# Optimization experiments

Measured on AMD Instinct MI355X. Metric: run time of the kernel, lower is better.

## Reference

```python
import jax, jax.numpy as jnp
import numpy as np

IN_DIM = 128
SLOT_SIZE = 64
NUM_SLOTS = 8
NUM_ITERS = 3
MLP_HDIM = 128
EPSILON = 1e-08


def _layernorm(x, g, b, eps=1e-5):
    m = jnp.mean(x, axis=-1, keepdims=True)
    v = jnp.mean((x - m) ** 2, axis=-1, keepdims=True)
    return (x - m) * jax.lax.rsqrt(v + eps) * g + b


def setup_inputs() -> dict:
    key = jax.random.key(0)
    ks = jax.random.split(key, 16)
    H, D, K, M = SLOT_SIZE, IN_DIM, NUM_SLOTS, MLP_HDIM
    x = jax.random.normal(ks[0], (32, 4096, D), dtype=jnp.float32)
    noise = jax.random.normal(ks[1], (32, K, H), dtype=jnp.float32)
    s = lambda k, shape, fan_in: jax.random.normal(k, shape, jnp.float32) * (1.0 / np.sqrt(fan_in))
    return {
        'x': x,
        'noise': noise,
        'Wq': s(ks[2], (H, H), H),            # project_q (no bias)
        'Wk': s(ks[3], (H, D), D),            # project_k
        'Wv': s(ks[4], (H, D), D),            # project_v
        'ln_in_g': jnp.ones((D,), jnp.float32), 'ln_in_b': jnp.zeros((D,), jnp.float32),
        'ln_sl_g': jnp.ones((H,), jnp.float32), 'ln_sl_b': jnp.zeros((H,), jnp.float32),
        'ln_mlp_g': jnp.ones((H,), jnp.float32), 'ln_mlp_b': jnp.zeros((H,), jnp.float32),
        'gru_w_ih': s(ks[5], (3 * H, H), H),  # PyTorch GRUCell weight_ih (r,z,n)
        'gru_w_hh': s(ks[6], (3 * H, H), H),
        'gru_b_ih': jnp.zeros((3 * H,), jnp.float32),
        'gru_b_hh': jnp.zeros((3 * H,), jnp.float32),
        'mlp_w1': s(ks[7], (M, H), H), 'mlp_b1': jnp.zeros((M,), jnp.float32),
        'mlp_w2': s(ks[8], (H, M), M), 'mlp_b2': jnp.zeros((H,), jnp.float32),
        'slots_mu': jnp.tile(jnp.linspace(-1.0, 1.0, K, dtype=jnp.float32)[None, :, None], (1, 1, H)),
        'slots_logsigma': jnp.full((1, K, H), -1.0, dtype=jnp.float32),
    }


def reference(x, noise, Wq, Wk, Wv, ln_in_g, ln_in_b, ln_sl_g, ln_sl_b,
              ln_mlp_g, ln_mlp_b, gru_w_ih, gru_w_hh, gru_b_ih, gru_b_hh,
              mlp_w1, mlp_b1, mlp_w2, mlp_b2, slots_mu, slots_logsigma):
    B = x.shape[0]
    H, K = SLOT_SIZE, NUM_SLOTS
    xn = _layernorm(x, ln_in_g, ln_in_b)
    k = jnp.einsum('bnd,hd->bnh', xn, Wk)  # [B,N,H]
    v = jnp.einsum('bnd,hd->bnh', xn, Wv)

    scale = jax.nn.softplus(slots_logsigma) + 1e-05
    slots = slots_mu + scale * noise  # rsample, broadcast over batch -> [B,K,H]

    def step(slots):
        slots_prev = slots
        s = _layernorm(slots, ln_sl_g, ln_sl_b)
        q = jnp.einsum('bkh,gh->bkg', s, Wq)  # [B,K,H]
        scores = (H ** -0.5) * jnp.einsum('bnh,bkh->bnk', k, q)
        attn = jax.nn.softmax(scores, axis=-1) + EPSILON  # softmax over slots
        attn = attn / jnp.sum(attn, axis=1, keepdims=True)  # normalize over inputs
        updates = jnp.einsum('bnk,bnh->bkh', attn, v)
        # PyTorch GRUCell: gates ordered (r, z, n)
        u = updates.reshape(-1, H)
        h = slots_prev.reshape(-1, H)
        gx = u @ gru_w_ih.T + gru_b_ih
        gh = h @ gru_w_hh.T + gru_b_hh
        xr, xz, xn_ = jnp.split(gx, 3, axis=-1)
        hr, hz, hn = jnp.split(gh, 3, axis=-1)
        r = jax.nn.sigmoid(xr + hr)
        z = jax.nn.sigmoid(xz + hz)
        n = jnp.tanh(xn_ + r * hn)
        slots = ((1.0 - z) * n + z * h).reshape(B, K, H)
        slots = _layernorm(slots, ln_mlp_g, ln_mlp_b)
        mlp_out = jax.nn.relu(slots @ mlp_w1.T + mlp_b1) @ mlp_w2.T + mlp_b2
        return slots + mlp_out

    for _ in range(NUM_ITERS):
        slots = step(slots)
    return slots
```

## Files before the change

kernel.cpp:

```cpp
#include <hip/hip_runtime.h>

typedef __attribute__((ext_vector_type(8))) short s16x8;
typedef __attribute__((ext_vector_type(4))) float f32x4;

#define DEV static __device__ __forceinline__

DEV float b2f(unsigned short u){
  unsigned int i = ((unsigned int)u) << 16;
  float f; __builtin_memcpy(&f, &i, 4); return f;
}
DEV unsigned short f2b(float f){
  unsigned int i; __builtin_memcpy(&i, &f, 4);
  i = i + 0x7fffu + ((i >> 16) & 1u);
  return (unsigned short)(i >> 16);
}
DEV f32x4 mfma16(s16x8 a, s16x8 b, f32x4 c){
  return __builtin_amdgcn_mfma_f32_16x16x32_bf16(a, b, c, 0, 0, 0);
}
DEV s16x8 ld8f(const float* p){
  const float4* q4 = (const float4*)p;
  float4 a = q4[0], b = q4[1];
  s16x8 r;
  r[0]=(short)f2b(a.x); r[1]=(short)f2b(a.y); r[2]=(short)f2b(a.z); r[3]=(short)f2b(a.w);
  r[4]=(short)f2b(b.x); r[5]=(short)f2b(b.y); r[6]=(short)f2b(b.z); r[7]=(short)f2b(b.w);
  return r;
}

template<int C> DEV float dpp_addstep(float x){
  int y = __builtin_amdgcn_update_dpp(0, __builtin_bit_cast(int, x), C, 0xF, 0xF, true);
  return x + __builtin_bit_cast(float, y);
}
DEV float rsum16(float v){
  v = dpp_addstep<0xB1>(v);
  v = dpp_addstep<0x4E>(v);
  v = dpp_addstep<0x141>(v);
  v = dpp_addstep<0x140>(v);
  return v;
}

__global__ __launch_bounds__(256) void k_wpack(
    const float* __restrict__ Wk, const float* __restrict__ Wv,
    unsigned short* __restrict__ wkb, unsigned short* __restrict__ wvb)
{
  int t = blockIdx.x * 256 + threadIdx.x;
  const float* src = (t < 2048) ? (Wk + t*4) : (Wv + (t-2048)*4);
  unsigned short* dst = (t < 2048) ? (wkb + t*4) : (wvb + (t-2048)*4);
  float4 v = *(const float4*)src;
  ushort4 o;
  o.x = f2b(v.x); o.y = f2b(v.y); o.z = f2b(v.z); o.w = f2b(v.w);
  *(ushort4*)dst = o;
}

__global__ __launch_bounds__(256, 4) void k_lnkv(
    const float* __restrict__ x,
    const unsigned short* __restrict__ wkb,
    const unsigned short* __restrict__ wvb,
    const float* __restrict__ lg,
    const float* __restrict__ lb,
    unsigned short* __restrict__ kg,
    unsigned short* __restrict__ vt)
{
  __shared__ unsigned int xs[128 * 68];
  const int tid = threadIdx.x;
  const int w = tid >> 6, ln = tid & 63;
  const int m16 = ln & 15, q = ln >> 4;
  const int b = blockIdx.x >> 5;
  const int nbase = (blockIdx.x & 31) << 7;
  const long rowg0 = (long)b * 4096 + nbase;

  {
    const int c = m16;
    const float4 gA = *(const float4*)(lg + c*4);
    const float4 gB = *(const float4*)(lg + 64 + c*4);
    const float4 bA = *(const float4*)(lb + c*4);
    const float4 bB = *(const float4*)(lb + 64 + c*4);
    const float* base = x + (rowg0 + w*32 + q)*128;

    float4 va[2], vb[2];
    va[0] = *(const float4*)(base + c*4);
    vb[0] = *(const float4*)(base + 64 + c*4);
    #pragma unroll
    for (int p = 0; p < 8; ++p){
      const int cur = p & 1, nxt = cur ^ 1;
      if (p < 7){
        va[nxt] = *(const float4*)(base + (p+1)*512 + c*4);
        vb[nxt] = *(const float4*)(base + (p+1)*512 + 64 + c*4);
      }
      float4 u = va[cur], t = vb[cur];
      float s1 = (u.x + u.y) + (u.z + u.w) + (t.x + t.y) + (t.z + t.w);
      float s2 = (u.x*u.x + u.y*u.y) + (u.z*u.z + u.w*u.w)
               + (t.x*t.x + t.y*t.y) + (t.z*t.z + t.w*t.w);
      s1 = rsum16(s1);
      s2 = rsum16(s2);
      float mean = s1 * (1.f/128.f);
      float var  = s2 * (1.f/128.f) - mean*mean;
      float rs = rsqrtf(var + 1e-5f);
      float y0 = (u.x - mean)*rs*gA.x + bA.x;
      float y1 = (u.y - mean)*rs*gA.y + bA.y;
      float y2 = (u.z - mean)*rs*gA.z + bA.z;
      float y3 = (u.w - mean)*rs*gA.w + bA.w;
      float y4 = (t.x - mean)*rs*gB.x + bB.x;
      float y5 = (t.y - mean)*rs*gB.y + bB.y;
      float y6 = (t.z - mean)*rs*gB.z + bB.z;
      float y7 = (t.w - mean)*rs*gB.w + bB.w;
      uint2 pkA, pkB;
      pkA.x = (unsigned int)f2b(y0) | ((unsigned int)f2b(y1) << 16);
      pkA.y = (unsigned int)f2b(y2) | ((unsigned int)f2b(y3) << 16);
      pkB.x = (unsigned int)f2b(y4) | ((unsigned int)f2b(y5) << 16);
      pkB.y = (unsigned int)f2b(y6) | ((unsigned int)f2b(y7) << 16);
      const int r = w*32 + p*4 + q;
      *(uint2*)&xs[r*68 + c*2] = pkA;
      *(uint2*)&xs[r*68 + 32 + c*2] = pkB;
    }
  }

  s16x8 bw[4][4];
  #pragma unroll
  for (int t = 0; t < 4; ++t)
    #pragma unroll
    for (int kb = 0; kb < 4; ++kb)
      bw[kb][t] = *(const s16x8*)(wkb + (t*16 + m16)*128 + kb*32 + q*8);

  __syncthreads();

  const f32x4 zf = {0.f, 0.f, 0.f, 0.f};

  #pragma unroll
  for (int mi = 0; mi < 2; ++mi){
    int n0 = (w*2 + mi) * 16;
    f32x4 acc[4];
    #pragma unroll
    for (int t = 0; t < 4; ++t) acc[t] = zf;
    #pragma unroll
    for (int kb = 0; kb < 4; ++kb){
      s16x8 af = *(const s16x8*)((const unsigned short*)(xs + (n0 + m16)*68) + kb*32 + q*8);
      #pragma unroll
      for (int t = 0; t < 4; ++t)
        acc[t] = mfma16(af, bw[kb][t], acc[t]);
    }
    #pragma unroll
    for (int t = 0; t < 4; ++t){
      int h = t*16 + m16;
      #pragma unroll
      for (int rr = 0; rr < 4; ++rr){
        long n = rowg0 + n0 + q*4 + rr;
        kg[n*64 + h] = f2b(acc[t][rr]);
      }
    }
  }

  #pragma unroll
  for (int t = 0; t < 4; ++t)
    #pragma unroll
    for (int kb = 0; kb < 4; ++kb)
      bw[kb][t] = *(const s16x8*)(wvb + (t*16 + m16)*128 + kb*32 + q*8);

  #pragma unroll
  for (int mi = 0; mi < 2; ++mi){
    int n0 = (w*2 + mi) * 16;
    f32x4 acc[4];
    #pragma unroll
    for (int t = 0; t < 4; ++t) acc[t] = zf;
    #pragma unroll
    for (int kb = 0; kb < 4; ++kb){
      s16x8 af = *(const s16x8*)((const unsigned short*)(xs + (n0 + m16)*68) + kb*32 + q*8);
      #pragma unroll
      for (int t = 0; t < 4; ++t)
        acc[t] = mfma16(af, bw[kb][t], acc[t]);
    }
    #pragma unroll
    for (int t = 0; t < 4; ++t){
      int h = t*16 + m16;
      unsigned int p0 = (unsigned int)f2b(acc[t][0]) | ((unsigned int)f2b(acc[t][1]) << 16);
      unsigned int p1 = (unsigned int)f2b(acc[t][2]) | ((unsigned int)f2b(acc[t][3]) << 16);
      uint2 pv; pv.x = p0; pv.y = p1;
      long off = ((long)b*64 + h)*4096 + nbase + n0 + q*4;
      *(uint2*)(vt + off) = pv;
    }
  }
}

__global__ __launch_bounds__(256) void k_init2(
    const float* __restrict__ noise,
    const float* __restrict__ mu,
    const float* __restrict__ lsg,
    const float* __restrict__ gsl,
    const float* __restrict__ bsl,
    const float* __restrict__ Wq,
    float* __restrict__ slots,
    unsigned short* __restrict__ qws,
    float* __restrict__ U, float* __restrict__ S)
{
  __shared__ unsigned short st[16*72];
  __shared__ __align__(16) float redS[16][4];
  __shared__ __align__(16) float redQ[16][4];
  const int tid = threadIdx.x;
  const int w = tid >> 6, ln = tid & 63;
  const int m16 = ln & 15, q = ln >> 4;
  const int r0 = blockIdx.x * 16;
  const int cw = w*16 + m16;

  float sl[4], s1[4], s2[4];
  #pragma unroll
  for (int rr = 0; rr < 4; ++rr){
    int row = r0 + q*4 + rr;
    int k = row & 7;
    float v = mu[k*64 + cw] + (log1pf(expf(lsg[k*64 + cw])) + 1e-5f) * noise[row*64 + cw];
    sl[rr] = v;
    slots[row*64 + cw] = v;
    s1[rr] = v; s2[rr] = v*v;
  }
  #pragma unroll
  for (int m = 1; m < 16; m <<= 1){
    #pragma unroll
    for (int rr = 0; rr < 4; ++rr){
      s1[rr] += __shfl_xor(s1[rr], m);
      s2[rr] += __shfl_xor(s2[rr], m);
    }
  }
  if (m16 == 0){
    #pragma unroll
    for (int rr = 0; rr < 4; ++rr){ redS[q*4+rr][w] = s1[rr]; redQ[q*4+rr][w] = s2[rr]; }
  }
  __syncthreads();
  {
    const float gs = gsl[cw], bs = bsl[cw];
    #pragma unroll
    for (int rr = 0; rr < 4; ++rr){
      f32x4 aS = *(const f32x4*)redS[q*4+rr];
      f32x4 aQ = *(const f32x4*)redQ[q*4+rr];
      float tS = aS[0]+aS[1]+aS[2]+aS[3];
      float tQ = aQ[0]+aQ[1]+aQ[2]+aQ[3];
      float mean = tS*(1.f/64.f);
      float var  = tQ*(1.f/64.f) - mean*mean;
      float rs = rsqrtf(var + 1e-5f);
      float sq = (sl[rr] - mean)*rs*gs + bs;
      st[(q*4+rr)*72 + cw] = f2b(sq);
    }
  }
  __syncthreads();
  {
    f32x4 acc = {0,0,0,0};
    #pragma unroll
    for (int ks = 0; ks < 2; ++ks){
      s16x8 a = *(const s16x8*)(st + m16*72 + ks*32 + q*8);
      acc = mfma16(a, ld8f(Wq + cw*64 + ks*32 + q*8), acc);
    }
    #pragma unroll
    for (int rr = 0; rr < 4; ++rr){
      int row = r0 + q*4 + rr;
      int bb_ = row >> 3, kk = row & 7;
      qws[(bb_*16 + kk)*64 + cw] = f2b(acc[rr] * 0.125f);
    }
  }
  {
    f32x4 z = {0,0,0,0};
    *(f32x4*)(U + r0*64 + tid*4) = z;
    if (tid < 16) S[r0 + tid] = 0.f;
    int b0 = blockIdx.x * 2;
    ((unsigned int*)(qws + (b0*16 + 8)*64))[tid] = 0u;
    ((unsigned int*)(qws + ((b0+1)*16 + 8)*64))[tid] = 0u;
  }
}

__global__ __launch_bounds__(256) void k_attn(
    const unsigned short* __restrict__ kg,
    const unsigned short* __restrict__ vt,
    const unsigned short* __restrict__ qws,
    float* __restrict__ U, float* __restrict__ S)
{
  __shared__ float sc[256*17];
  __shared__ unsigned short aT[16*264];
  const int tid = threadIdx.x;
  const int w = tid >> 6, ln = tid & 63;
  const int m16 = ln & 15, q = ln >> 4;
  const int b = blockIdx.x >> 4;
  const int nbase = (blockIdx.x & 15) << 8;

  for (int i = tid; i < 8*264; i += 256) aT[8*264 + i] = 0;

  s16x8 bq[2];
  #pragma unroll
  for (int ks = 0; ks < 2; ++ks)
    bq[ks] = *(const s16x8*)(qws + (b*16 + m16)*64 + ks*32 + q*8);

  #pragma unroll
  for (int mi = 0; mi < 4; ++mi){
    int n0 = (w*4 + mi)*16;
    f32x4 acc = {0.f, 0.f, 0.f, 0.f};
    #pragma unroll
    for (int ks = 0; ks < 2; ++ks){
      s16x8 af = *(const s16x8*)(kg + ((long)b*4096 + nbase + n0 + m16)*64 + ks*32 + q*8);
      acc = mfma16(af, bq[ks], acc);
    }
    #pragma unroll
    for (int rr = 0; rr < 4; ++rr)
      sc[(n0 + q*4 + rr)*17 + m16] = acc[rr];
  }
  __syncthreads();

  {
    int r = tid;
    float a8[8];
    float mx = -1e30f;
    #pragma unroll
    for (int j = 0; j < 8; ++j){ a8[j] = sc[r*17 + j]; mx = fmaxf(mx, a8[j]); }
    float ssum = 0.f;
    #pragma unroll
    for (int j = 0; j < 8; ++j){ a8[j] = expf(a8[j] - mx); ssum += a8[j]; }
    float inv = 1.f/ssum;
    #pragma unroll
    for (int j = 0; j < 8; ++j)
      aT[j*264 + r] = f2b(a8[j]*inv + 1e-8f);
  }
  __syncthreads();

  {
    int j = tid >> 5, c = tid & 31;
    float p = 0.f;
    #pragma unroll
    for (int i = 0; i < 8; ++i) p += b2f(aT[j*264 + c + 32*i]);
    #pragma unroll
    for (int m = 16; m >= 1; m >>= 1) p += __shfl_xor(p, m);
    if ((ln & 31) == 0) atomicAdd(&S[b*8 + j], p);
  }

  {
    f32x4 acc = {0.f, 0.f, 0.f, 0.f};
    #pragma unroll
    for (int ks = 0; ks < 8; ++ks){
      s16x8 af = *(const s16x8*)(aT + m16*264 + ks*32 + q*8);
      s16x8 bf = *(const s16x8*)(vt + ((long)b*64 + w*16 + m16)*4096 + nbase + ks*32 + q*8);
      acc = mfma16(af, bf, acc);
    }
    #pragma unroll
    for (int rr = 0; rr < 4; ++rr){
      int slot = q*4 + rr;
      if (slot < 8)
        atomicAdd(&U[b*512 + slot*64 + w*16 + m16], acc[rr]);
    }
  }
}

__global__ __launch_bounds__(256) void k_gru(
    const float* __restrict__ U, const float* __restrict__ S,
    float* __restrict__ slots,
    const float* __restrict__ wih, const float* __restrict__ whh,
    const float* __restrict__ bih, const float* __restrict__ bhh,
    const float* __restrict__ w1, const float* __restrict__ b1p,
    const float* __restrict__ w2, const float* __restrict__ b2p,
    const float* __restrict__ gmlp, const float* __restrict__ bmlp,
    const float* __restrict__ gsl, const float* __restrict__ bsl,
    const float* __restrict__ Wq,
    unsigned short* __restrict__ qws,
    float* __restrict__ outp,
    float* __restrict__ Uz, float* __restrict__ Sz)
{
  __shared__ unsigned short ut[16*72], ht[16*72], st[16*72], hid[16*136];
  __shared__ __align__(16) float redS[16][4];
  __shared__ __align__(16) float redQ[16][4];
  const int tid = threadIdx.x;
  const int w = tid >> 6, ln = tid & 63;
  const int m16 = ln & 15, q = ln >> 4;
  const int r0 = blockIdx.x * 16;
  const int cw = w*16 + m16;

  #pragma unroll
  for (int p = 0; p < 4; ++p){
    int row = p*4 + w;
    float sv = S[r0 + row];
    float uu = U[(r0 + row)*64 + ln] / sv;
    ut[row*72 + ln] = f2b(uu);
    ht[row*72 + ln] = f2b(slots[(r0 + row)*64 + ln]);
  }
  __syncthreads();

  f32x4 axr = {0,0,0,0}, axz = {0,0,0,0}, axn = {0,0,0,0};
  f32x4 ahr = {0,0,0,0}, ahz = {0,0,0,0}, ahn = {0,0,0,0};
  #pragma unroll
  for (int ks = 0; ks < 2; ++ks){
    s16x8 au = *(const s16x8*)(ut + m16*72 + ks*32 + q*8);
    s16x8 ah = *(const s16x8*)(ht + m16*72 + ks*32 + q*8);
    axr = mfma16(au, ld8f(wih + (      cw)*64 + ks*32 + q*8), axr);
    axz = mfma16(au, ld8f(wih + ( 64 + cw)*64 + ks*32 + q*8), axz);
    axn = mfma16(au, ld8f(wih + (128 + cw)*64 + ks*32 + q*8), axn);
    ahr = mfma16(ah, ld8f(whh + (      cw)*64 + ks*32 + q*8), ahr);
    ahz = mfma16(ah, ld8f(whh + ( 64 + cw)*64 + ks*32 + q*8), ahz);
    ahn = mfma16(ah, ld8f(whh + (128 + cw)*64 + ks*32 + q*8), ahn);
  }
  const float bxr = bih[cw], bxz = bih[64+cw], bxn = bih[128+cw];
  const float bhr = bhh[cw], bhz = bhh[64+cw], bhn = bhh[128+cw];
  float sp[4];
  #pragma unroll
  for (int rr = 0; rr < 4; ++rr){
    float xr = axr[rr] + bxr, xz = axz[rr] + bxz, xnv = axn[rr] + bxn;
    float hr = ahr[rr] + bhr, hz = ahz[rr] + bhz, hn = ahn[rr] + bhn;
    float rg = 1.f / (1.f + expf(-(xr + hr)));
    float zg = 1.f / (1.f + expf(-(xz + hz)));
    float ng = tanhf(xnv + rg*hn);
    float hv = b2f(ht[(q*4 + rr)*72 + cw]);
    sp[rr] = (1.f - zg)*ng + zg*hv;
  }

  float s1[4], s2[4];
  #pragma unroll
  for (int rr = 0; rr < 4; ++rr){ s1[rr] = sp[rr]; s2[rr] = sp[rr]*sp[rr]; }
  #pragma unroll
  for (int m = 1; m < 16; m <<= 1){
    #pragma unroll
    for (int rr = 0; rr < 4; ++rr){
      s1[rr] += __shfl_xor(s1[rr], m);
      s2[rr] += __shfl_xor(s2[rr], m);
    }
  }
  if (m16 == 0){
    #pragma unroll
    for (int rr = 0; rr < 4; ++rr){ redS[q*4+rr][w] = s1[rr]; redQ[q*4+rr][w] = s2[rr]; }
  }
  __syncthreads();
  float sl_[4];
  {
    const float gm = gmlp[cw], bm = bmlp[cw];
    #pragma unroll
    for (int rr = 0; rr < 4; ++rr){
      f32x4 aS = *(const f32x4*)redS[q*4+rr];
      f32x4 aQ = *(const f32x4*)redQ[q*4+rr];
      float tS = aS[0]+aS[1]+aS[2]+aS[3];
      float tQ = aQ[0]+aQ[1]+aQ[2]+aQ[3];
      float mean = tS*(1.f/64.f);
      float var  = tQ*(1.f/64.f) - mean*mean;
      float rs = rsqrtf(var + 1e-5f);
      sl_[rr] = (sp[rr] - mean)*rs*gm + bm;
      st[(q*4+rr)*72 + cw] = f2b(sl_[rr]);
    }
  }
  __syncthreads();

  #pragma unroll
  for (int t2 = 0; t2 < 2; ++t2){
    int nt = w*2 + t2;
    int col = nt*16 + m16;
    f32x4 acc = {0,0,0,0};
    #pragma unroll
    for (int ks = 0; ks < 2; ++ks){
      s16x8 a = *(const s16x8*)(st + m16*72 + ks*32 + q*8);
      acc = mfma16(a, ld8f(w1 + col*64 + ks*32 + q*8), acc);
    }
    float bb = b1p[col];
    #pragma unroll
    for (int rr = 0; rr < 4; ++rr)
      hid[(q*4+rr)*136 + col] = f2b(fmaxf(acc[rr] + bb, 0.f));
  }
  __syncthreads();

  float snew[4];
  {
    f32x4 acc = {0,0,0,0};
    #pragma unroll
    for (int ks = 0; ks < 4; ++ks){
      s16x8 a = *(const s16x8*)(hid + m16*136 + ks*32 + q*8);
      acc = mfma16(a, ld8f(w2 + cw*128 + ks*32 + q*8), acc);
    }
    float bb = b2p[cw];
    #pragma unroll
    for (int rr = 0; rr < 4; ++rr){
      snew[rr] = sl_[rr] + acc[rr] + bb;
      int row = r0 + q*4 + rr;
      slots[row*64 + cw] = snew[rr];
      outp[row*64 + cw] = snew[rr];
    }
  }

  #pragma unroll
  for (int rr = 0; rr < 4; ++rr){ s1[rr] = snew[rr]; s2[rr] = snew[rr]*snew[rr]; }
  #pragma unroll
  for (int m = 1; m < 16; m <<= 1){
    #pragma unroll
    for (int rr = 0; rr < 4; ++rr){
      s1[rr] += __shfl_xor(s1[rr], m);
      s2[rr] += __shfl_xor(s2[rr], m);
    }
  }
  __syncthreads();
  if (m16 == 0){
    #pragma unroll
    for (int rr = 0; rr < 4; ++rr){ redS[q*4+rr][w] = s1[rr]; redQ[q*4+rr][w] = s2[rr]; }
  }
  __syncthreads();
  {
    const float gs = gsl[cw], bs = bsl[cw];
    #pragma unroll
    for (int rr = 0; rr < 4; ++rr){
      f32x4 aS = *(const f32x4*)redS[q*4+rr];
      f32x4 aQ = *(const f32x4*)redQ[q*4+rr];
      float tS = aS[0]+aS[1]+aS[2]+aS[3];
      float tQ = aQ[0]+aQ[1]+aQ[2]+aQ[3];
      float mean = tS*(1.f/64.f);
      float var  = tQ*(1.f/64.f) - mean*mean;
      float rs = rsqrtf(var + 1e-5f);
      float sq = (snew[rr] - mean)*rs*gs + bs;
      st[(q*4+rr)*72 + cw] = f2b(sq);
    }
  }
  __syncthreads();
  {
    f32x4 acc = {0,0,0,0};
    #pragma unroll
    for (int ks = 0; ks < 2; ++ks){
      s16x8 a = *(const s16x8*)(st + m16*72 + ks*32 + q*8);
      acc = mfma16(a, ld8f(Wq + cw*64 + ks*32 + q*8), acc);
    }
    #pragma unroll
    for (int rr = 0; rr < 4; ++rr){
      int row = r0 + q*4 + rr;
      int bb_ = row >> 3, kk = row & 7;
      qws[(bb_*16 + kk)*64 + cw] = f2b(acc[rr] * 0.125f);
    }
  }
  {
    f32x4 z = {0,0,0,0};
    *(f32x4*)(Uz + r0*64 + tid*4) = z;
    if (tid < 16) Sz[r0 + tid] = 0.f;
    int b0 = blockIdx.x * 2;
    unsigned int* qp0 = (unsigned int*)(qws + (b0*16 + 8)*64);
    unsigned int* qp1 = (unsigned int*)(qws + ((b0+1)*16 + 8)*64);
    qp0[tid] = 0u;
    qp1[tid] = 0u;
  }
}

extern "C" void kernel_launch(void* const* d_in, const int* in_sizes, int n_in,
                              void* d_out, int out_size, void* d_ws, size_t ws_size,
                              hipStream_t stream)
{
  const float* x    = (const float*)d_in[0];
  const float* noise= (const float*)d_in[1];
  const float* Wq   = (const float*)d_in[2];
  const float* Wk   = (const float*)d_in[3];
  const float* Wv   = (const float*)d_in[4];
  const float* ling = (const float*)d_in[5];
  const float* linb = (const float*)d_in[6];
  const float* gsl  = (const float*)d_in[7];
  const float* bsl  = (const float*)d_in[8];
  const float* gmlp = (const float*)d_in[9];
  const float* bmlp = (const float*)d_in[10];
  const float* wih  = (const float*)d_in[11];
  const float* whh  = (const float*)d_in[12];
  const float* bih  = (const float*)d_in[13];
  const float* bhh  = (const float*)d_in[14];
  const float* w1   = (const float*)d_in[15];
  const float* b1p  = (const float*)d_in[16];
  const float* w2   = (const float*)d_in[17];
  const float* b2p  = (const float*)d_in[18];
  const float* mu   = (const float*)d_in[19];
  const float* lsg  = (const float*)d_in[20];

  char* ws = (char*)d_ws;
  unsigned short* kg   = (unsigned short*)(ws);
  unsigned short* vt   = (unsigned short*)(ws + 16777216);
  unsigned short* qws  = (unsigned short*)(ws + 33554432);
  float* slots         = (float*)(ws + 33619968);
  float* U             = (float*)(ws + 33685504);
  float* S             = (float*)(ws + 33751040);
  unsigned short* wkb  = (unsigned short*)(ws + 33752064);
  unsigned short* wvb  = (unsigned short*)(ws + 33768448);
  float* outp          = (float*)d_out;

  hipLaunchKernelGGL(k_wpack, dim3(16), dim3(256), 0, stream, Wk, Wv, wkb, wvb);
  hipLaunchKernelGGL(k_lnkv, dim3(1024), dim3(256), 0, stream, x, wkb, wvb, ling, linb, kg, vt);
  hipLaunchKernelGGL(k_init2, dim3(16), dim3(256), 0, stream, noise, mu, lsg, gsl, bsl, Wq, slots, qws, U, S);
  for (int it = 0; it < 3; ++it){
    hipLaunchKernelGGL(k_attn, dim3(512), dim3(256), 0, stream, kg, vt, qws, U, S);
    hipLaunchKernelGGL(k_gru, dim3(16), dim3(256), 0, stream, U, S, slots,
                       wih, whh, bih, bhh, w1, b1p, w2, b2p, gmlp, bmlp, gsl, bsl, Wq,
                       qws, outp, U, S);
  }
  (void)in_sizes; (void)n_in; (void)out_size; (void)ws_size;
}
```

Measured before the change: 220.0 us.

## Fuse GRU/MLP slot update into attention kernel prologue, drop intermediate GRU launches

Each attention block now recomputes the GRU, MLP, layernorm and q-projection for its batch pair from the previous iteration's U/S accumulators. This replaces the separate 16-block k_gru launches between iterations. Triple-buffered U/S and slot buffers avoid zeroing races, and all small weights are prepacked to bf16 in k_wpack. The trade is redundant per-block compute (32 blocks per batch pair repeat the same work) and extra LDS, in exchange for fewer launches and fewer serial low-occupancy kernels.

Measured after the change: 209.2 us. 1.05x faster.

```diff
diff --git a/kernel.cpp b/kernel.cpp
--- a/kernel.cpp
+++ b/kernel.cpp
@@ -40,11 +40,22 @@
 
 __global__ __launch_bounds__(256) void k_wpack(
     const float* __restrict__ Wk, const float* __restrict__ Wv,
-    unsigned short* __restrict__ wkb, unsigned short* __restrict__ wvb)
+    const float* __restrict__ wih, const float* __restrict__ whh,
+    const float* __restrict__ w1, const float* __restrict__ w2,
+    const float* __restrict__ Wq,
+    unsigned short* __restrict__ wkb, unsigned short* __restrict__ wvb,
+    unsigned short* __restrict__ wall)
 {
   int t = blockIdx.x * 256 + threadIdx.x;
-  const float* src = (t < 2048) ? (Wk + t*4) : (Wv + (t-2048)*4);
-  unsigned short* dst = (t < 2048) ? (wkb + t*4) : (wvb + (t-2048)*4);
+  int off = t * 4;
+  const float* src; unsigned short* dst;
+  if      (off <  8192){ src = Wk  + off;         dst = wkb  + off; }
+  else if (off < 16384){ src = Wv  + off -  8192; dst = wvb  + off - 8192; }
+  else if (off < 28672){ src = wih + off - 16384; dst = wall + off - 16384; }
+  else if (off < 40960){ src = whh + off - 28672; dst = wall + off - 16384; }
+  else if (off < 49152){ src = w1  + off - 40960; dst = wall + off - 16384; }
+  else if (off < 57344){ src = w2  + off - 49152; dst = wall + off - 16384; }
+  else                 { src = Wq  + off - 57344; dst = wall + off - 16384; }
   float4 v = *(const float4*)src;
   ushort4 o;
   o.x = f2b(v.x); o.y = f2b(v.y); o.z = f2b(v.z); o.w = f2b(v.w);
@@ -189,7 +200,8 @@
     const float* __restrict__ Wq,
     float* __restrict__ slots,
     unsigned short* __restrict__ qws,
-    float* __restrict__ U, float* __restrict__ S)
+    float* __restrict__ U0, float* __restrict__ U1, float* __restrict__ U2,
+    float* __restrict__ S0, float* __restrict__ S1, float* __restrict__ S2)
 {
   __shared__ unsigned short st[16*72];
   __shared__ __align__(16) float redS[16][4];
@@ -255,22 +267,37 @@
   }
   {
     f32x4 z = {0,0,0,0};
-    *(f32x4*)(U + r0*64 + tid*4) = z;
-    if (tid < 16) S[r0 + tid] = 0.f;
+    *(f32x4*)(U0 + r0*64 + tid*4) = z;
+    *(f32x4*)(U1 + r0*64 + tid*4) = z;
+    *(f32x4*)(U2 + r0*64 + tid*4) = z;
+    if (tid < 16){ S0[r0 + tid] = 0.f; S1[r0 + tid] = 0.f; S2[r0 + tid] = 0.f; }
     int b0 = blockIdx.x * 2;
     ((unsigned int*)(qws + (b0*16 + 8)*64))[tid] = 0u;
     ((unsigned int*)(qws + ((b0+1)*16 + 8)*64))[tid] = 0u;
   }
 }
 
-__global__ __launch_bounds__(256) void k_attn(
+__global__ __launch_bounds__(256) void k_attn2(
     const unsigned short* __restrict__ kg,
     const unsigned short* __restrict__ vt,
     const unsigned short* __restrict__ qws,
-    float* __restrict__ U, float* __restrict__ S)
+    const unsigned short* __restrict__ wall,
+    const float* __restrict__ bih, const float* __restrict__ bhh,
+    const float* __restrict__ b1p, const float* __restrict__ b2p,
+    const float* __restrict__ gmlp, const float* __restrict__ bmlp,
+    const float* __restrict__ gsl, const float* __restrict__ bsl,
+    const float* __restrict__ Uin, const float* __restrict__ Sin,
+    float* __restrict__ Uout, float* __restrict__ Sout,
+    const float* __restrict__ slin, float* __restrict__ slout,
+    int it)
 {
   __shared__ float sc[256*17];
   __shared__ unsigned short aT[16*264];
+  __shared__ unsigned short ut[16*72], ht[16*72], st[16*72], hid[16*136];
+  __shared__ unsigned short qloc[16*72];
+  __shared__ __align__(16) float redS[16][4];
+  __shared__ __align__(16) float redQ[16][4];
+
   const int tid = threadIdx.x;
   const int w = tid >> 6, ln = tid & 63;
   const int m16 = ln & 15, q = ln >> 4;
@@ -278,11 +305,184 @@
   const int nbase = (blockIdx.x & 15) << 8;
 
   for (int i = tid; i < 8*264; i += 256) aT[8*264 + i] = 0;
+  if (tid < 128){
+    int row = 8 + (tid >> 4), c = (tid & 15)*4;
+    ushort4 z4 = {0,0,0,0};
+    *(ushort4*)&qloc[row*72 + c] = z4;
+  }
+
+  if (it == 0){
+    if (tid < 128){
+      int row = tid >> 4, c = (tid & 15)*4;
+      *(ushort4*)&qloc[row*72 + c] = *(const ushort4*)(qws + (b*16 + row)*64 + c);
+    }
+  } else {
+    const int r0 = (b >> 1) * 16;
+    const int cw = w*16 + m16;
+    const unsigned short* wihb = wall;
+    const unsigned short* whhb = wall + 12288;
+    const unsigned short* w1b  = wall + 24576;
+    const unsigned short* w2b  = wall + 32768;
+    const unsigned short* wqb  = wall + 40960;
+
+    #pragma unroll
+    for (int p = 0; p < 4; ++p){
+      int row = p*4 + w;
+      float sv = Sin[r0 + row];
+      float uu = Uin[(r0 + row)*64 + ln] / sv;
+      ut[row*72 + ln] = f2b(uu);
+      ht[row*72 + ln] = f2b(slin[(r0 + row)*64 + ln]);
+    }
+    __syncthreads();
+
+    f32x4 axr = {0,0,0,0}, axz = {0,0,0,0}, axn = {0,0,0,0};
+    f32x4 ahr = {0,0,0,0}, ahz = {0,0,0,0}, ahn = {0,0,0,0};
+    #pragma unroll
+    for (int ks = 0; ks < 2; ++ks){
+      s16x8 au = *(const s16x8*)(ut + m16*72 + ks*32 + q*8);
+      s16x8 ah = *(const s16x8*)(ht + m16*72 + ks*32 + q*8);
+      axr = mfma16(au, *(const s16x8*)(wihb + (      cw)*64 + ks*32 + q*8), axr);
+      axz = mfma16(au, *(const s16x8*)(wihb + ( 64 + cw)*64 + ks*32 + q*8), axz);
+      axn = mfma16(au, *(const s16x8*)(wihb + (128 + cw)*64 + ks*32 + q*8), axn);
+      ahr = mfma16(ah, *(const s16x8*)(whhb + (      cw)*64 + ks*32 + q*8), ahr);
+      ahz = mfma16(ah, *(const s16x8*)(whhb + ( 64 + cw)*64 + ks*32 + q*8), ahz);
+      ahn = mfma16(ah, *(const s16x8*)(whhb + (128 + cw)*64 + ks*32 + q*8), ahn);
+    }
+    const float bxr = bih[cw], bxz = bih[64+cw], bxn = bih[128+cw];
+    const float bhr = bhh[cw], bhz = bhh[64+cw], bhn = bhh[128+cw];
+    float sp[4];
+    #pragma unroll
+    for (int rr = 0; rr < 4; ++rr){
+      float xr = axr[rr] + bxr, xz = axz[rr] + bxz, xnv = axn[rr] + bxn;
+      float hr = ahr[rr] + bhr, hz = ahz[rr] + bhz, hn = ahn[rr] + bhn;
+      float rg = 1.f / (1.f + expf(-(xr + hr)));
+      float zg = 1.f / (1.f + expf(-(xz + hz)));
+      float ng = tanhf(xnv + rg*hn);
+      float hv = b2f(ht[(q*4 + rr)*72 + cw]);
+      sp[rr] = (1.f - zg)*ng + zg*hv;
+    }
+
+    float s1[4], s2[4];
+    #pragma unroll
+    for (int rr = 0; rr < 4; ++rr){ s1[rr] = sp[rr]; s2[rr] = sp[rr]*sp[rr]; }
+    #pragma unroll
+    for (int m = 1; m < 16; m <<= 1){
+      #pragma unroll
+      for (int rr = 0; rr < 4; ++rr){
+        s1[rr] += __shfl_xor(s1[rr], m);
+        s2[rr] += __shfl_xor(s2[rr], m);
+      }
+    }
+    if (m16 == 0){
+      #pragma unroll
+      for (int rr = 0; rr < 4; ++rr){ redS[q*4+rr][w] = s1[rr]; redQ[q*4+rr][w] = s2[rr]; }
+    }
+    __syncthreads();
+    float sl_[4];
+    {
+      const float gm = gmlp[cw], bm = bmlp[cw];
+      #pragma unroll
+      for (int rr = 0; rr < 4; ++rr){
+        f32x4 aS = *(const f32x4*)redS[q*4+rr];
+        f32x4 aQ = *(const f32x4*)redQ[q*4+rr];
+        float tS = aS[0]+aS[1]+aS[2]+aS[3];
+        float tQ = aQ[0]+aQ[1]+aQ[2]+aQ[3];
+        float mean = tS*(1.f/64.f);
+        float var  = tQ*(1.f/64.f) - mean*mean;
+        float rs = rsqrtf(var + 1e-5f);
+        sl_[rr] = (sp[rr] - mean)*rs*gm + bm;
+        st[(q*4+rr)*72 + cw] = f2b(sl_[rr]);
+      }
+    }
+    __syncthreads();
+
+    #pragma unroll
+    for (int t2 = 0; t2 < 2; ++t2){
+      int nt = w*2 + t2;
+      int col = nt*16 + m16;
+      f32x4 acc = {0,0,0,0};
+      #pragma unroll
+      for (int ks = 0; ks < 2; ++ks){
+        s16x8 a = *(const s16x8*)(st + m16*72 + ks*32 + q*8);
+        acc = mfma16(a, *(const s16x8*)(w1b + col*64 + ks*32 + q*8), acc);
+      }
+      float bb = b1p[col];
+      #pragma unroll
+      for (int rr = 0; rr < 4; ++rr)
+        hid[(q*4+rr)*136 + col] = f2b(fmaxf(acc[rr] + bb, 0.f));
+    }
+    __syncthreads();
+
+    float snew[4];
+    {
+      f32x4 acc = {0,0,0,0};
+      #pragma unroll
+      for (int ks = 0; ks < 4; ++ks){
+        s16x8 a = *(const s16x8*)(hid + m16*136 + ks*32 + q*8);
+        acc = mfma16(a, *(const s16x8*)(w2b + cw*128 + ks*32 + q*8), acc);
+      }
+      float bb = b2p[cw];
+      #pragma unroll
+      for (int rr = 0; rr < 4; ++rr){
+        snew[rr] = sl_[rr] + acc[rr] + bb;
+        if ((blockIdx.x & 31) == 0)
+          slout[(r0 + q*4 + rr)*64 + cw] = snew[rr];
+      }
+    }
+
+    #pragma unroll
+    for (int rr = 0; rr < 4; ++rr){ s1[rr] = snew[rr]; s2[rr] = snew[rr]*snew[rr]; }
+    #pragma unroll
+    for (int m = 1; m < 16; m <<= 1){
+      #pragma unroll
+      for (int rr = 0; rr < 4; ++rr){
+        s1[rr] += __shfl_xor(s1[rr], m);
+        s2[rr] += __shfl_xor(s2[rr], m);
+      }
+    }
+    __syncthreads();
+    if (m16 == 0){
+      #pragma unroll
+      for (int rr = 0; rr < 4; ++rr){ redS[q*4+rr][w] = s1[rr]; redQ[q*4+rr][w] = s2[rr]; }
+    }
+    __syncthreads();
+    {
+      const float gs = gsl[cw], bs = bsl[cw];
+      #pragma unroll
+      for (int rr = 0; rr < 4; ++rr){
+        f32x4 aS = *(const f32x4*)redS[q*4+rr];
+        f32x4 aQ = *(const f32x4*)redQ[q*4+rr];
+        float tS = aS[0]+aS[1]+aS[2]+aS[3];
+        float tQ = aQ[0]+aQ[1]+aQ[2]+aQ[3];
+        float mean = tS*(1.f/64.f);
+        float var  = tQ*(1.f/64.f) - mean*mean;
+        float rs = rsqrtf(var + 1e-5f);
+        float sq = (snew[rr] - mean)*rs*gs + bs;
+        st[(q*4+rr)*72 + cw] = f2b(sq);
+      }
+    }
+    __syncthreads();
+    {
+      f32x4 acc = {0,0,0,0};
+      #pragma unroll
+      for (int ks = 0; ks < 2; ++ks){
+        s16x8 a = *(const s16x8*)(st + m16*72 + ks*32 + q*8);
+        acc = mfma16(a, *(const s16x8*)(wqb + cw*64 + ks*32 + q*8), acc);
+      }
+      #pragma unroll
+      for (int rr = 0; rr < 4; ++rr){
+        int rloc = q*4 + rr;
+        if ((rloc >> 3) == (b & 1))
+          qloc[(rloc & 7)*72 + cw] = f2b(acc[rr] * 0.125f);
+      }
+    }
+  }
+  __syncthreads();
 
   s16x8 bq[2];
   #pragma unroll
   for (int ks = 0; ks < 2; ++ks)
-    bq[ks] = *(const s16x8*)(qws + (b*16 + m16)*64 + ks*32 + q*8);
+    bq[ks] = *(const s16x8*)(qloc + m16*72 + ks*32 + q*8);
 
   #pragma unroll
   for (int mi = 0; mi < 4; ++mi){
@@ -322,7 +522,7 @@
     for (int i = 0; i < 8; ++i) p += b2f(aT[j*264 + c + 32*i]);
     #pragma unroll
     for (int m = 16; m >= 1; m >>= 1) p += __shfl_xor(p, m);
-    if ((ln & 31) == 0) atomicAdd(&S[b*8 + j], p);
+    if ((ln & 31) == 0) atomicAdd(&Sout[b*8 + j], p);
   }
 
   {
@@ -337,7 +537,7 @@
     for (int rr = 0; rr < 4; ++rr){
       int slot = q*4 + rr;
       if (slot < 8)
-        atomicAdd(&U[b*512 + slot*64 + w*16 + m16], acc[rr]);
+        atomicAdd(&Uout[b*512 + slot*64 + w*16 + m16], acc[rr]);
     }
   }
 }
@@ -350,11 +550,7 @@
     const float* __restrict__ w1, const float* __restrict__ b1p,
     const float* __restrict__ w2, const float* __restrict__ b2p,
     const float* __restrict__ gmlp, const float* __restrict__ bmlp,
-    const float* __restrict__ gsl, const float* __restrict__ bsl,
-    const float* __restrict__ Wq,
-    unsigned short* __restrict__ qws,
-    float* __restrict__ outp,
-    float* __restrict__ Uz, float* __restrict__ Sz)
+    float* __restrict__ outp)
 {
   __shared__ unsigned short ut[16*72], ht[16*72], st[16*72], hid[16*136];
   __shared__ __align__(16) float redS[16][4];
@@ -453,7 +649,6 @@
   }
   __syncthreads();
 
-  float snew[4];
   {
     f32x4 acc = {0,0,0,0};
     #pragma unroll
@@ -464,68 +659,9 @@
     float bb = b2p[cw];
     #pragma unroll
     for (int rr = 0; rr < 4; ++rr){
-      snew[rr] = sl_[rr] + acc[rr] + bb;
       int row = r0 + q*4 + rr;
-      slots[row*64 + cw] = snew[rr];
-      outp[row*64 + cw] = snew[rr];
-    }
-  }
-
-  #pragma unroll
-  for (int rr = 0; rr < 4; ++rr){ s1[rr] = snew[rr]; s2[rr] = snew[rr]*snew[rr]; }
-  #pragma unroll
-  for (int m = 1; m < 16; m <<= 1){
-    #pragma unroll
-    for (int rr = 0; rr < 4; ++rr){
-      s1[rr] += __shfl_xor(s1[rr], m);
-      s2[rr] += __shfl_xor(s2[rr], m);
-    }
-  }
-  __syncthreads();
-  if (m16 == 0){
-    #pragma unroll
-    for (int rr = 0; rr < 4; ++rr){ redS[q*4+rr][w] = s1[rr]; redQ[q*4+rr][w] = s2[rr]; }
-  }
-  __syncthreads();
-  {
-    const float gs = gsl[cw], bs = bsl[cw];
-    #pragma unroll
-    for (int rr = 0; rr < 4; ++rr){
-      f32x4 aS = *(const f32x4*)redS[q*4+rr];
-      f32x4 aQ = *(const f32x4*)redQ[q*4+rr];
-      float tS = aS[0]+aS[1]+aS[2]+aS[3];
-      float tQ = aQ[0]+aQ[1]+aQ[2]+aQ[3];
-      float mean = tS*(1.f/64.f);
-      float var  = tQ*(1.f/64.f) - mean*mean;
-      float rs = rsqrtf(var + 1e-5f);
-      float sq = (snew[rr] - mean)*rs*gs + bs;
-      st[(q*4+rr)*72 + cw] = f2b(sq);
-    }
-  }
-  __syncthreads();
-  {
-    f32x4 acc = {0,0,0,0};
-    #pragma unroll
-    for (int ks = 0; ks < 2; ++ks){
-      s16x8 a = *(const s16x8*)(st + m16*72 + ks*32 + q*8);
-      acc = mfma16(a, ld8f(Wq + cw*64 + ks*32 + q*8), acc);
-    }
-    #pragma unroll
-    for (int rr = 0; rr < 4; ++rr){
-      int row = r0 + q*4 + rr;
-      int bb_ = row >> 3, kk = row & 7;
-      qws[(bb_*16 + kk)*64 + cw] = f2b(acc[rr] * 0.125f);
-    }
-  }
-  {
-    f32x4 z = {0,0,0,0};
-    *(f32x4*)(Uz + r0*64 + tid*4) = z;
-    if (tid < 16) Sz[r0 + tid] = 0.f;
-    int b0 = blockIdx.x * 2;
-    unsigned int* qp0 = (unsigned int*)(qws + (b0*16 + 8)*64);
-    unsigned int* qp1 = (unsigned int*)(qws + ((b0+1)*16 + 8)*64);
-    qp0[tid] = 0u;
-    qp1[tid] = 0u;
+      outp[row*64 + cw] = sl_[rr] + acc[rr] + bb;
+    }
   }
 }
 
@@ -558,22 +694,37 @@
   char* ws = (char*)d_ws;
   unsigned short* kg   = (unsigned short*)(ws);
   unsigned short* vt   = (unsigned short*)(ws + 16777216);
-  unsigned short* qws  = (unsigned short*)(ws + 33554432);
-  float* slots         = (float*)(ws + 33619968);
-  float* U             = (float*)(ws + 33685504);
-  float* S             = (float*)(ws + 33751040);
-  unsigned short* wkb  = (unsigned short*)(ws + 33752064);
-  unsigned short* wvb  = (unsigned short*)(ws + 33768448);
+  char* base = ws + 33554432;
+  unsigned short* qws  = (unsigned short*)(base);
+  float* slotsA        = (float*)(base + 65536);
+  float* slotsB        = (float*)(base + 131072);
+  float* slotsC        = (float*)(base + 196608);
+  float* U0            = (float*)(base + 262144);
+  float* U1            = (float*)(base + 327680);
+  float* U2            = (float*)(base + 393216);
+  float* S0            = (float*)(base + 458752);
+  float* S1            = (float*)(base + 459776);
+  float* S2            = (float*)(base + 460800);
+  unsigned short* wkb  = (unsigned short*)(base + 461824);
+  unsigned short* wvb  = (unsigned short*)(base + 478208);
+  unsigned short* wall = (unsigned short*)(base + 494592);
   float* outp          = (float*)d_out;
 
-  hipLaunchKernelGGL(k_wpack, dim3(16), dim3(256), 0, stream, Wk, Wv, wkb, wvb);
+  hipLaunchKernelGGL(k_wpack, dim3(60), dim3(256), 0, stream,
+                     Wk, Wv, wih, whh, w1, w2, Wq, wkb, wvb, wall);
   hipLaunchKernelGGL(k_lnkv, dim3(1024), dim3(256), 0, stream, x, wkb, wvb, ling, linb, kg, vt);
-  hipLaunchKernelGGL(k_init2, dim3(16), dim3(256), 0, stream, noise, mu, lsg, gsl, bsl, Wq, slots, qws, U, S);
-  for (int it = 0; it < 3; ++it){
-    hipLaunchKernelGGL(k_attn, dim3(512), dim3(256), 0, stream, kg, vt, qws, U, S);
-    hipLaunchKernelGGL(k_gru, dim3(16), dim3(256), 0, stream, U, S, slots,
-                       wih, whh, bih, bhh, w1, b1p, w2, b2p, gmlp, bmlp, gsl, bsl, Wq,
-                       qws, outp, U, S);
-  }
+  hipLaunchKernelGGL(k_init2, dim3(16), dim3(256), 0, stream,
+                     noise, mu, lsg, gsl, bsl, Wq, slotsA, qws, U0, U1, U2, S0, S1, S2);
+  hipLaunchKernelGGL(k_attn2, dim3(512), dim3(256), 0, stream,
+                     kg, vt, qws, wall, bih, bhh, b1p, b2p, gmlp, bmlp, gsl, bsl,
+                     U0, S0, U0, S0, slotsA, slotsA, 0);
+  hipLaunchKernelGGL(k_attn2, dim3(512), dim3(256), 0, stream,
+                     kg, vt, qws, wall, bih, bhh, b1p, b2p, gmlp, bmlp, gsl, bsl,
+                     U0, S0, U1, S1, slotsA, slotsB, 1);
+  hipLaunchKernelGGL(k_attn2, dim3(512), dim3(256), 0, stream,
+                     kg, vt, qws, wall, bih, bhh, b1p, b2p, gmlp, bmlp, gsl, bsl,
+                     U1, S1, U2, S2, slotsB, slotsC, 2);
+  hipLaunchKernelGGL(k_gru, dim3(16), dim3(256), 0, stream, U2, S2, slotsC,
+                     wih, whh, bih, bhh, w1, b1p, w2, b2p, gmlp, bmlp, outp);
   (void)in_sizes; (void)n_in; (void)out_size; (void)ws_size;
 }
```
